# Kernel tuning notes

Measured on AMD Instinct MI355X. Metric: run time of the kernel, lower is better.

The kernel has to match this reference:

```python
import jax, jax.numpy as jnp
import numpy as np

B, C, H, W = 2, 256, 64, 64
CQ = C // 8  # query/key channels in PAM


def setup_inputs() -> dict:
    key = jax.random.key(0)
    ks = jax.random.split(key, 16)
    s = lambda *sh: sh
    inp = {
        'r_f': jax.random.normal(ks[0], (B, C, H, W), jnp.float32),
        'g_f': jax.random.normal(ks[1], (B, C, H, W), jnp.float32),
        'b_f': jax.random.normal(ks[2], (B, C, H, W), jnp.float32),
        'a_f': jax.random.normal(ks[3], (B, C, H, W), jnp.float32),
        # PAM params (1x1 convs)
        'Wq': jax.random.normal(ks[4], (CQ, C), jnp.float32) * (2.0 / C) ** 0.5,
        'bq': jnp.zeros((CQ,), jnp.float32),
        'Wk': jax.random.normal(ks[5], (CQ, C), jnp.float32) * (2.0 / C) ** 0.5,
        'bk': jnp.zeros((CQ,), jnp.float32),
        'Wv': jax.random.normal(ks[6], (C, C), jnp.float32) * (2.0 / C) ** 0.5,
        'bv': jnp.zeros((C,), jnp.float32),
        'gamma_pam': jax.random.normal(ks[7], (1,), jnp.float32) * 0.1,
        'gamma_cam': jax.random.normal(ks[8], (1,), jnp.float32) * 0.1,
        # 3x3 conv (shared across the 4 streams)
        'Wd': jax.random.normal(ks[9], (C, C, 3, 3), jnp.float32) * (2.0 / (C * 9)) ** 0.5,
        'bd': jnp.zeros((C,), jnp.float32),
    }
    return inp


def _pam(x, Wq, bq, Wk, bk, Wv, bv, gamma):
    # x: [B,C,H,W]
    b, c, h, w = x.shape
    n = h * w
    q = jnp.einsum('oc,bchw->bohw', Wq, x) + bq[None, :, None, None]  # [B,CQ,H,W]
    k = jnp.einsum('oc,bchw->bohw', Wk, x) + bk[None, :, None, None]
    v = jnp.einsum('oc,bchw->bohw', Wv, x) + bv[None, :, None, None]  # [B,C,H,W]
    q = q.reshape(b, -1, n)  # [B,CQ,N]
    k = k.reshape(b, -1, n)
    v = v.reshape(b, c, n)
    energy = jnp.einsum('bcn,bcm->bnm', q, k)            # [B,N,N]
    att = jax.nn.softmax(energy, axis=-1)
    out = jnp.einsum('bcm,bnm->bcn', v, att).reshape(b, c, h, w)
    return gamma * out + x


def _cam_att(x):
    b, c, h, w = x.shape
    v = x.reshape(b, c, h * w)
    energy = jnp.einsum('bcn,bdn->bcd', v, v)            # [B,C,C]
    energy_new = jnp.max(energy, axis=-1, keepdims=True) - energy
    return jax.nn.softmax(energy_new, axis=-1)


def _forward(r_f, g_f, b_f, a_f, Wq, bq, Wk, bk, Wv, bv, gamma_pam, gamma_cam, Wd, bd):
    xs = jnp.stack([r_f, g_f, b_f, a_f])                 # [4,B,C,H,W]
    s, b, c, h, w = xs.shape
    n = h * w
    sp = jax.vmap(lambda x: _pam(x, Wq, bq, Wk, bk, Wv, bv, gamma_pam))(xs)
    att = jax.vmap(_cam_att)(xs)                         # [4,B,C,C]
    # Each stream s accumulates cam_use(x_s, att_t) over all 4 attentions t:
    # sum_t (gamma*att_t@V_s + x_s) = gamma*(sum_t att_t)@V_s + 4*x_s
    att_sum = att.sum(axis=0)                            # [B,C,C]
    V = xs.reshape(s, b, c, n)
    sc = gamma_cam * jnp.einsum('bcd,sbdn->sbcn', att_sum, V).reshape(s, b, c, h, w) + 4.0 * xs
    y = sp + sc                                          # [4,B,C,H,W]
    y = y.reshape(s * b, c, h, w)
    y = jax.lax.conv_general_dilated(y, Wd, (1, 1), 'SAME',
                                     dimension_numbers=('NCHW', 'OIHW', 'NCHW'))
    y = y + bd[None, :, None, None]
    y = y.reshape(s, b, c, h, w)
    return (y[0], y[1], y[2], y[3])


def reference(r_f, g_f, b_f, a_f, Wq, bq, Wk, bk, Wv, bv, gamma_pam, gamma_cam, Wd, bd):
    return _forward(r_f, g_f, b_f, a_f, Wq, bq, Wk, bk, Wv, bv, gamma_pam, gamma_cam, Wd, bd)
```

## Files before the change

### kernel.cpp

```cpp
#include <hip/hip_runtime.h>


#define HW 4096

typedef unsigned short u16;
typedef __attribute__((ext_vector_type(4))) float f32x4;
typedef __attribute__((ext_vector_type(8))) short bf16x8;
typedef __attribute__((ext_vector_type(4))) unsigned u32x4;
typedef __attribute__((ext_vector_type(8))) unsigned short u16x8;
typedef __attribute__((ext_vector_type(4))) unsigned short u16x4;

__device__ __forceinline__ float bf2f(u16 u) { return __uint_as_float(((unsigned)u) << 16); }
__device__ __forceinline__ u16 f2bf(float f) {
    unsigned x = __float_as_uint(f);
    return (u16)((x + 0x7fffu + ((x >> 16) & 1u)) >> 16);
}
__device__ __forceinline__ void gload16(const void* g, void* l) {
    __builtin_amdgcn_global_load_lds((const __attribute__((address_space(1))) void*)g,
                                     (__attribute__((address_space(3))) void*)l, 16, 0, 0);
}
__device__ __forceinline__ unsigned cvtpk(float lo, float hi) {
    unsigned r;
    asm("v_cvt_pk_bf16_f32 %0, %1, %2" : "=v"(r) : "v"(lo), "v"(hi));
    return r;
}

struct XPtrs { const float* p[4]; };

enum { PM_QK = 0, PM_V = 1, PM_CAM = 2, PM_CONV = 3 };

template<int MODE>
__global__ __launch_bounds__(256)
void mfma_p_k(const u16* __restrict__ A, const u16* __restrict__ Bp,
              void* __restrict__ Cp,
              const float* __restrict__ b0, const float* __restrict__ b1,
              const float* __restrict__ gscale, XPtrs xs,
              int K, int lda, long aBatch, long bBatch, long cBatch, int sb0)
{
    const int n0 = blockIdx.x * 128, m0 = blockIdx.y * 128, z = blockIdx.z;
    const u16* Ab = A + (MODE == PM_CAM ? (size_t)(z & 1) * aBatch : (size_t)z * aBatch)
                      + (size_t)m0 * lda;
    const u16* Bb = Bp + (size_t)z * bBatch + (size_t)n0 * 8;

    __shared__ u16 As[4096];
    __shared__ u16 Bs[4096];

    const int t = threadIdx.x, lane = t & 63, w = t >> 6;
    const int mw = (w >> 1) * 64, nw = (w & 1) * 64;
    const int l15 = lane & 15, l4 = lane >> 4;

    f32x4 acc[4][4] = {};

    const u16* gaw = Ab + (size_t)lane * lda + w * 8;
    const u16* gbw = Bb + (size_t)w * (HW * 8) + (size_t)lane * 8;

    for (int kb = 0; kb < K; kb += 32) {
        gload16(gaw + kb,                    &As[w * 1024]);
        gload16(gaw + kb + (size_t)64 * lda, &As[w * 1024 + 512]);
        const u16* gb = gbw + (size_t)(kb >> 3) * (HW * 8);
        gload16(gb,       &Bs[w * 1024]);
        gload16(gb + 512, &Bs[w * 1024 + 512]);
        __syncthreads();

        bf16x8 af[4], bf[4];
        #pragma unroll
        for (int i = 0; i < 4; ++i) {
            af[i] = *(const bf16x8*)&As[l4 * 1024 + (mw + i * 16 + l15) * 8];
            bf[i] = *(const bf16x8*)&Bs[l4 * 1024 + (nw + i * 16 + l15) * 8];
        }
        #pragma unroll
        for (int mi = 0; mi < 4; ++mi)
            #pragma unroll
            for (int ni = 0; ni < 4; ++ni)
                acc[mi][ni] = __builtin_amdgcn_mfma_f32_16x16x32_bf16(af[mi], bf[ni], acc[mi][ni], 0, 0, 0);
        __syncthreads();
    }

    #pragma unroll
    for (int mi = 0; mi < 4; ++mi) {
        #pragma unroll
        for (int ni = 0; ni < 4; ++ni) {
            #pragma unroll
            for (int r = 0; r < 4; ++r) {
                const int row = m0 + mw + mi * 16 + l4 * 4 + r;
                const int col = n0 + nw + ni * 16 + l15;
                float v = acc[mi][ni][r];
                if constexpr (MODE == PM_QK) {
                    if (row < 64) {
                        v += (row < 32) ? b0[row] : b1[row - 32];
                        ((u16*)Cp)[(size_t)z * cBatch + (size_t)row * HW + col] = f2bf(v);
                    }
                } else if constexpr (MODE == PM_V) {
                    v += b0[row];
                    ((u16*)Cp)[(size_t)z * cBatch
                               + (((size_t)(col >> 3) * 256 + row) << 3) + (col & 7)] = f2bf(v);
                } else if constexpr (MODE == PM_CAM) {
                    const float* xb = xs.p[z >> 1] + (size_t)(z & 1) * (256 * HW);
                    v = gscale[0] * v + 5.f * xb[(size_t)row * HW + col];
                    ((float*)Cp)[(size_t)z * cBatch + (size_t)row * HW + col] = v;
                } else {
                    v += b0[row];
                    ((float*)Cp)[(size_t)(sb0 + z) * cBatch + (size_t)row * HW + col] = v;
                }
            }
        }
    }
}

__global__ __launch_bounds__(512, 4)
void flash_k(const u16* __restrict__ QKt, const u16* __restrict__ Vp,
             float* __restrict__ Yt, const float* __restrict__ gscale)
{
    __shared__ u16 Vs[32768];

    const int sb = blockIdx.y;
    const int t = threadIdx.x, w = t >> 6, lane = t & 63;
    const int l15 = lane & 15, l4 = lane >> 4;
    const int q0 = blockIdx.x * 128 + w * 16;

    const u16* QKb = QKt + (size_t)sb * ((size_t)HW * 64);
    const u16* Vb  = Vp + (size_t)sb * ((size_t)256 * HW);
    float* Yb = Yt + (size_t)sb * ((size_t)HW * 256);

    const bf16x8 aq = *(const bf16x8*)&QKb[(size_t)(q0 + l15) * 64 + l4 * 8];

    f32x4 acc[16] = {};
    float lrun = 0.f;
    const f32x4 zero4 = {0.f, 0.f, 0.f, 0.f};

    const int idxA = (l15 + ((lane & 16) << 1)) << 2;
    const int idxB = idxA + (16 << 2);
    const bool jhi = (lane & 32) != 0;

    for (int it = 0; it < 32; ++it) {
        __syncthreads();

        const u16* vsrc = Vb + (size_t)it * 32768;
        #pragma unroll
        for (int i = 0; i < 8; ++i)
            gload16(vsrc + i * 4096 + t * 8, &Vs[i * 4096 + t * 8]);

        const int m0 = it * 128;
        unsigned pk[16];
        float tsum = 0.f;
        #pragma unroll
        for (int j = 0; j < 8; ++j) {
            const bf16x8 bk = *(const bf16x8*)&QKb[(size_t)(m0 + j * 16 + l15) * 64 + 32 + l4 * 8];
            const f32x4 sj = __builtin_amdgcn_mfma_f32_16x16x32_bf16(bk, aq, zero4, 0, 0, 0);
            const float e0 = __expf(sj[0]);
            const float e1 = __expf(sj[1]);
            const float e2 = __expf(sj[2]);
            const float e3 = __expf(sj[3]);
            tsum += (e0 + e1) + (e2 + e3);
            pk[2 * j]     = cvtpk(e0, e1);
            pk[2 * j + 1] = cvtpk(e2, e3);
        }
        tsum += __shfl_xor(tsum, 16);
        tsum += __shfl_xor(tsum, 32);
        lrun += tsum;

        __syncthreads();

        #pragma unroll
        for (int ks = 0; ks < 4; ++ks) {
            u32x4 D;
            {
                const unsigned a0 = __builtin_amdgcn_ds_bpermute(idxA, (int)pk[4 * ks + 0]);
                const unsigned b0_ = __builtin_amdgcn_ds_bpermute(idxA, (int)pk[4 * ks + 2]);
                D[0] = jhi ? b0_ : a0;
                const unsigned a1 = __builtin_amdgcn_ds_bpermute(idxA, (int)pk[4 * ks + 1]);
                const unsigned b1_ = __builtin_amdgcn_ds_bpermute(idxA, (int)pk[4 * ks + 3]);
                D[1] = jhi ? b1_ : a1;
                const unsigned a2 = __builtin_amdgcn_ds_bpermute(idxB, (int)pk[4 * ks + 0]);
                const unsigned b2_ = __builtin_amdgcn_ds_bpermute(idxB, (int)pk[4 * ks + 2]);
                D[2] = jhi ? b2_ : a2;
                const unsigned a3 = __builtin_amdgcn_ds_bpermute(idxB, (int)pk[4 * ks + 1]);
                const unsigned b3_ = __builtin_amdgcn_ds_bpermute(idxB, (int)pk[4 * ks + 3]);
                D[3] = jhi ? b3_ : a3;
            }
            const bf16x8 ap = __builtin_bit_cast(bf16x8, D);
            #pragma unroll
            for (int ct = 0; ct < 16; ++ct) {
                const bf16x8 bv = *(const bf16x8*)&Vs[(4 * ks + l4) * 2048 + (ct * 16 + l15) * 8];
                acc[ct] = __builtin_amdgcn_mfma_f32_16x16x32_bf16(ap, bv, acc[ct], 0, 0, 0);
            }
        }
    }

    const float gp = gscale[0];
    #pragma unroll
    for (int r = 0; r < 4; ++r) {
        const int srcl = ((lane & 48) | (l4 * 4 + r)) << 2;
        const float lr = __int_as_float(__builtin_amdgcn_ds_bpermute(srcl, __float_as_int(lrun)));
        const float sc = gp / lr;
        const int row = q0 + l4 * 4 + r;
        #pragma unroll
        for (int ct = 0; ct < 16; ++ct)
            Yb[(size_t)row * 256 + ct * 16 + l15] = acc[ct][r] * sc;
    }
}

__global__ __launch_bounds__(256)
void xpack_k(XPtrs xs, u16* __restrict__ Xp)
{
    __shared__ float tile[64][65];
    const int sb = blockIdx.z;
    const int n0 = blockIdx.x * 64, c0 = blockIdx.y * 64;
    const float* X = xs.p[sb >> 1] + (size_t)(sb & 1) * (256 * HW);
    u16* Xo = Xp + (size_t)sb * ((size_t)32 * HW * 8);
    const int t = threadIdx.x;
    {
        const int c = t >> 2, p = t & 3;
        const float4* s4 = (const float4*)&X[(size_t)(c0 + c) * HW + n0 + p * 16];
        #pragma unroll
        for (int i = 0; i < 4; ++i) {
            const float4 v = s4[i];
            tile[c][p * 16 + i * 4 + 0] = v.x;
            tile[c][p * 16 + i * 4 + 1] = v.y;
            tile[c][p * 16 + i * 4 + 2] = v.z;
            tile[c][p * 16 + i * 4 + 3] = v.w;
        }
    }
    __syncthreads();
    const int n = t >> 2;
    #pragma unroll
    for (int pp = 0; pp < 2; ++pp) {
        const int cg = (t & 3) * 2 + pp;
        u16 o[8];
        #pragma unroll
        for (int cl = 0; cl < 8; ++cl) o[cl] = f2bf(tile[cg * 8 + cl][n]);
        *(u16x8*)&Xo[(((size_t)(c0 >> 3) + cg) * HW + (n0 + n)) * 8] = *(u16x8*)o;
    }
}

__global__ __launch_bounds__(256)
void tqkT_k(const u16* __restrict__ src, u16* __restrict__ dst)
{
    __shared__ u16 tile[64][72];
    const int sb = blockIdx.y;
    const int n0 = blockIdx.x * 64;
    const u16* s = src + (size_t)sb * (64 * HW);
    u16* d = dst + (size_t)sb * (HW * 64);
    const int t = threadIdx.x;
    #pragma unroll
    for (int p = 0; p < 2; ++p) {
        const int c = (t >> 3) + p * 32, nn = (t & 7) * 8;
        const u16x8 v = *(const u16x8*)&s[(size_t)c * HW + n0 + nn];
        *(u16x8*)&tile[c][nn] = v;
    }
    __syncthreads();
    const int n = t >> 2, co = (t & 3) * 16;
    u16 o[16];
    #pragma unroll
    for (int j = 0; j < 16; ++j) o[j] = tile[co + j][n];
    *(u16x8*)&d[(size_t)(n0 + n) * 64 + co]     = *(u16x8*)&o[0];
    *(u16x8*)&d[(size_t)(n0 + n) * 64 + co + 8] = *(u16x8*)&o[8];
}

__global__ __launch_bounds__(256)
void gram_k(float* __restrict__ Gp, XPtrs xs)
{
    const int bx = blockIdx.x, by = blockIdx.y, bz = blockIdx.z;
    const int sbi = bz & 7;
    const int n0 = bx * 64, m0 = by * 64;
    const int t = threadIdx.x;
    const int tm = t >> 4, tn = t & 15;
    const float* xb = xs.p[sbi >> 1] + (size_t)(sbi & 1) * (256 * HW) + (bz >> 3) * 512;

    __shared__ float As[16][68];
    __shared__ float Bs[16][68];
    float acc[4][4] = {};

    for (int kb = 0; kb < 512; kb += 16) {
        {
            const int m = t >> 2, k0 = (t & 3) * 4;
            float4 v = *(const float4*)(xb + (size_t)(m0 + m) * HW + (kb + k0));
            As[k0 + 0][m] = v.x; As[k0 + 1][m] = v.y; As[k0 + 2][m] = v.z; As[k0 + 3][m] = v.w;
        }
        {
            const int n = t >> 2, k0 = (t & 3) * 4;
            float4 v = *(const float4*)(xb + (size_t)(n0 + n) * HW + (kb + k0));
            Bs[k0 + 0][n] = v.x; Bs[k0 + 1][n] = v.y; Bs[k0 + 2][n] = v.z; Bs[k0 + 3][n] = v.w;
        }
        __syncthreads();
        #pragma unroll
        for (int k = 0; k < 16; ++k) {
            const float4 a = *(const float4*)&As[k][tm * 4];
            const float4 b = *(const float4*)&Bs[k][tn * 4];
            acc[0][0] += a.x * b.x; acc[0][1] += a.x * b.y; acc[0][2] += a.x * b.z; acc[0][3] += a.x * b.w;
            acc[1][0] += a.y * b.x; acc[1][1] += a.y * b.y; acc[1][2] += a.y * b.z; acc[1][3] += a.y * b.w;
            acc[2][0] += a.z * b.x; acc[2][1] += a.z * b.y; acc[2][2] += a.z * b.z; acc[2][3] += a.z * b.w;
            acc[3][0] += a.w * b.x; acc[3][1] += a.w * b.y; acc[3][2] += a.w * b.z; acc[3][3] += a.w * b.w;
        }
        __syncthreads();
    }
    float* Cf = Gp + (size_t)bz * 65536;
    #pragma unroll
    for (int i = 0; i < 4; ++i) {
        const int m = m0 + tm * 4 + i;
        *(float4*)&Cf[(size_t)m * 256 + n0 + tn * 4] =
            make_float4(acc[i][0], acc[i][1], acc[i][2], acc[i][3]);
    }
}

__global__ __launch_bounds__(256)
void greduce_k(const float* __restrict__ Gp, float* __restrict__ G)
{
    const size_t i = (size_t)blockIdx.x * 256 + threadIdx.x;
    float s = 0.f;
    #pragma unroll
    for (int sp = 0; sp < 8; ++sp) s += Gp[(size_t)sp * 524288 + i];
    G[i] = s;
}

__global__ __launch_bounds__(256)
void cam_softmax_k(const float* __restrict__ G, float* __restrict__ attsum)
{
    __shared__ float rmn[4], rsm[4];
    const int c = blockIdx.x, b = blockIdx.y;
    const int d = threadIdx.x;
    float acc = 0.f;
    for (int s = 0; s < 4; ++s) {
        const float* row = G + (((size_t)(s * 2 + b)) * 256 + c) * 256;
        const float e = row[d];
        float mn = e;
        for (int o = 32; o; o >>= 1) mn = fminf(mn, __shfl_down(mn, o));
        if ((d & 63) == 0) rmn[d >> 6] = mn;
        __syncthreads();
        mn = fminf(fminf(rmn[0], rmn[1]), fminf(rmn[2], rmn[3]));
        const float ex = __expf(mn - e);
        float sm = ex;
        for (int o = 32; o; o >>= 1) sm += __shfl_down(sm, o);
        if ((d & 63) == 0) rsm[d >> 6] = sm;
        __syncthreads();
        sm = rsm[0] + rsm[1] + rsm[2] + rsm[3];
        acc += ex * (1.0f / sm);
        __syncthreads();
    }
    attsum[((size_t)b * 256 + c) * 256 + d] = acc;
}

__global__ __launch_bounds__(256)
void transT_k(const float* __restrict__ Yt, float* __restrict__ Y)
{
    __shared__ float tile[64][65];
    const int sb = blockIdx.z;
    const int n0 = blockIdx.x * 64, c0 = blockIdx.y * 64;
    const float* src = Yt + (size_t)sb * ((size_t)HW * 256);
    float* dst = Y + (size_t)sb * ((size_t)256 * HW);
    const int t = threadIdx.x;
    {
        const int n = t >> 2, p = t & 3;
        const float4* s4 = (const float4*)&src[(size_t)(n0 + n) * 256 + c0 + p * 16];
        #pragma unroll
        for (int i = 0; i < 4; ++i) {
            const float4 v = s4[i];
            tile[n][p * 16 + i * 4 + 0] = v.x;
            tile[n][p * 16 + i * 4 + 1] = v.y;
            tile[n][p * 16 + i * 4 + 2] = v.z;
            tile[n][p * 16 + i * 4 + 3] = v.w;
        }
    }
    __syncthreads();
    const int c = t >> 2, p = t & 3;
    #pragma unroll
    for (int i = 0; i < 4; ++i) {
        float* dp = &dst[(size_t)(c0 + c) * HW + n0 + p * 16 + i * 4];
        float4 cur = *(float4*)dp;
        cur.x += tile[p * 16 + i * 4 + 0][c];
        cur.y += tile[p * 16 + i * 4 + 1][c];
        cur.z += tile[p * 16 + i * 4 + 2][c];
        cur.w += tile[p * 16 + i * 4 + 3][c];
        *(float4*)dp = cur;
    }
}

__global__ __launch_bounds__(256)
void im2col_k(const float* __restrict__ Y, u16* __restrict__ col, int sb0)
{
    const int n = blockIdx.x * 256 + threadIdx.x;
    const int kg = blockIdx.y;
    const int sbl = blockIdx.z;
    const float* Yb = Y + (size_t)(sb0 + sbl) * ((size_t)256 * HW);
    const int h = n >> 6, wc = n & 63;
    u16 out[8];
    #pragma unroll
    for (int kl = 0; kl < 8; ++kl) {
        const int k = kg * 8 + kl;
        const int ic = k / 9, r = k - ic * 9;
        const int ih = h + r / 3 - 1, iw = wc + (r % 3) - 1;
        float v = 0.f;
        if (ih >= 0 && ih < 64 && iw >= 0 && iw < 64)
            v = Yb[(size_t)ic * HW + (ih << 6) + iw];
        out[kl] = f2bf(v);
    }
    *(u16x8*)&col[(((size_t)sbl * 288 + kg) * HW + n) * 8] = *(u16x8*)out;
}

__global__ __launch_bounds__(256)
void cvt_k(const float* __restrict__ s, u16* __restrict__ d)
{
    const size_t i = ((size_t)blockIdx.x * 256 + threadIdx.x) * 4;
    const float4 v = *(const float4*)&s[i];
    u16 o[4] = { f2bf(v.x), f2bf(v.y), f2bf(v.z), f2bf(v.w) };
    *(u16x4*)&d[i] = *(u16x4*)o;
}

extern "C" void kernel_launch(void* const* d_in, const int* in_sizes, int n_in,
                              void* d_out, int out_size, void* d_ws, size_t ws_size,
                              hipStream_t stream)
{
    XPtrs xs;
    xs.p[0] = (const float*)d_in[0];
    xs.p[1] = (const float*)d_in[1];
    xs.p[2] = (const float*)d_in[2];
    xs.p[3] = (const float*)d_in[3];
    const float* Wq = (const float*)d_in[4];
    const float* bq = (const float*)d_in[5];
    const float* Wk = (const float*)d_in[6];
    const float* bk = (const float*)d_in[7];
    const float* Wv = (const float*)d_in[8];
    const float* bv = (const float*)d_in[9];
    const float* gp = (const float*)d_in[10];
    const float* gc = (const float*)d_in[11];
    const float* Wd = (const float*)d_in[12];
    const float* bd = (const float*)d_in[13];

    char* base = (char*)d_ws;
    size_t off = 0;
    auto alloc = [&](size_t bytes) -> char* {
        char* p = base + off;
        off = (off + bytes + 255) & ~(size_t)255;
        return p;
    };

    float* Y    = (float*)alloc((size_t)8 * 256 * HW * 4);
    u16*   Wdh  = (u16*)  alloc((size_t)256 * 2304 * 2);
    const size_t overlayStart = off;
    u16*   Xp   = (u16*)  alloc((size_t)8 * 32 * HW * 8 * 2);
    u16*   Vp   = (u16*)  alloc((size_t)8 * 256 * HW * 2);
    float* Yt   = (float*)alloc((size_t)8 * HW * 256 * 4);
    u16*   QKc  = (u16*)  alloc((size_t)8 * 64 * HW * 2);
    u16*   QKt  = (u16*)  alloc((size_t)8 * HW * 64 * 2);
    float* Gp   = (float*)alloc((size_t)64 * 65536 * 4);
    float* G    = (float*)alloc((size_t)8 * 65536 * 4);
    float* att  = (float*)alloc((size_t)2 * 65536 * 4);
    u16*   attH = (u16*)  alloc((size_t)2 * 65536 * 2);
    u16*   Wqkh = (u16*)  alloc((size_t)128 * 256 * 2);
    u16*   Wvh  = (u16*)  alloc((size_t)256 * 256 * 2);

    const size_t colPer = (size_t)288 * HW * 8 * 2;
    u16* colp = (u16*)(base + overlayStart);
    long nchunkL = (long)((ws_size - overlayStart) / colPer);
    const int nchunk = (int)(nchunkL > 8 ? 8 : (nchunkL < 1 ? 1 : nchunkL));

    dim3 T(256);

    xpack_k<<<dim3(64, 4, 8), T, 0, stream>>>(xs, Xp);
    cvt_k<<<dim3(8),   T, 0, stream>>>(Wq, Wqkh);
    cvt_k<<<dim3(8),   T, 0, stream>>>(Wk, Wqkh + 32 * 256);
    cvt_k<<<dim3(64),  T, 0, stream>>>(Wv, Wvh);
    cvt_k<<<dim3(576), T, 0, stream>>>(Wd, Wdh);

    gram_k<<<dim3(4, 4, 64), T, 0, stream>>>(Gp, xs);
    greduce_k<<<dim3(2048), T, 0, stream>>>(Gp, G);
    cam_softmax_k<<<dim3(256, 2), T, 0, stream>>>(G, att);
    cvt_k<<<dim3(128), T, 0, stream>>>(att, attH);

    mfma_p_k<PM_QK><<<dim3(32, 1, 8), T, 0, stream>>>(Wqkh, Xp, QKc, bq, bk, nullptr, xs,
                                                      256, 256, 0, (long)32 * HW * 8, (long)64 * HW, 0);
    tqkT_k<<<dim3(64, 8), T, 0, stream>>>(QKc, QKt);
    mfma_p_k<PM_V><<<dim3(32, 2, 8), T, 0, stream>>>(Wvh, Xp, Vp, bv, nullptr, nullptr, xs,
                                                     256, 256, 0, (long)32 * HW * 8, (long)256 * HW, 0);

    flash_k<<<dim3(32, 8), dim3(512), 0, stream>>>(QKt, Vp, Yt, gp);

    mfma_p_k<PM_CAM><<<dim3(32, 2, 8), T, 0, stream>>>(attH, Xp, Y, nullptr, nullptr, gc, xs,
                                                       256, 256, 65536, (long)32 * HW * 8, (long)256 * HW, 0);

    transT_k<<<dim3(64, 4, 8), T, 0, stream>>>(Yt, Y);

    for (int c0 = 0; c0 < 8; c0 += nchunk) {
        const int cs = (8 - c0 < nchunk) ? (8 - c0) : nchunk;
        im2col_k<<<dim3(16, 288, cs), T, 0, stream>>>(Y, colp, c0);
        mfma_p_k<PM_CONV><<<dim3(32, 2, cs), T, 0, stream>>>(Wdh, colp, d_out, bd, nullptr, nullptr, xs,
                                                             2304, 2304, 0, (long)288 * HW * 8, (long)256 * HW, c0);
    }
}
```

Measured before the change: 460.6 us.

## Compute CAM Gram matrix with split-bf16 MFMA instead of FP32 FMA

Replaces the scalar FP32 Gram kernel with an MFMA kernel that uses hi/lo bf16 splits (three products) to approximate FP32 accuracy. The split operands are produced by xpack in a K-major packed layout and reuse the V buffer's memory. This moves the main cost of the channel Gram computation onto the matrix cores, at the price of extra bytes written in xpack and slightly reduced precision from dropping the lo*lo term.

```diff
diff --git a/kernel.cpp b/kernel.cpp
--- a/kernel.cpp
+++ b/kernel.cpp
@@ -107,6 +107,71 @@
     }
 }
 
+__global__ __launch_bounds__(256)
+void gramm_k(const u16* __restrict__ Hi, const u16* __restrict__ Lo,
+             float* __restrict__ Gp)
+{
+    const int n0 = blockIdx.x * 128, m0 = blockIdx.y * 128, bz = blockIdx.z;
+    const int sb = bz & 7, sp = bz >> 3;
+    const u16* Hb = Hi + (size_t)sb * 1048576;
+    const u16* Lb = Lo + (size_t)sb * 1048576;
+
+    __shared__ u16 AsH[4096], AsL[4096], BsH[4096], BsL[4096];
+
+    const int t = threadIdx.x, lane = t & 63, w = t >> 6;
+    const int mw = (w >> 1) * 64, nw = (w & 1) * 64;
+    const int l15 = lane & 15, l4 = lane >> 4;
+
+    f32x4 acc[4][4] = {};
+
+    for (int kb = sp * 512; kb < sp * 512 + 512; kb += 32) {
+        const size_t g = (size_t)(kb >> 3) + w;
+        const u16* hA = Hb + g * 2048 + (size_t)(m0 + lane) * 8;
+        const u16* lA = Lb + g * 2048 + (size_t)(m0 + lane) * 8;
+        const u16* hB = Hb + g * 2048 + (size_t)(n0 + lane) * 8;
+        const u16* lB = Lb + g * 2048 + (size_t)(n0 + lane) * 8;
+        gload16(hA,       &AsH[w * 1024]);
+        gload16(hA + 512, &AsH[w * 1024 + 512]);
+        gload16(lA,       &AsL[w * 1024]);
+        gload16(lA + 512, &AsL[w * 1024 + 512]);
+        gload16(hB,       &BsH[w * 1024]);
+        gload16(hB + 512, &BsH[w * 1024 + 512]);
+        gload16(lB,       &BsL[w * 1024]);
+        gload16(lB + 512, &BsL[w * 1024 + 512]);
+        __syncthreads();
+
+        bf16x8 ah[4], al[4], bh[4], bl[4];
+        #pragma unroll
+        for (int i = 0; i < 4; ++i) {
+            ah[i] = *(const bf16x8*)&AsH[l4 * 1024 + (mw + i * 16 + l15) * 8];
+            al[i] = *(const bf16x8*)&AsL[l4 * 1024 + (mw + i * 16 + l15) * 8];
+            bh[i] = *(const bf16x8*)&BsH[l4 * 1024 + (nw + i * 16 + l15) * 8];
+            bl[i] = *(const bf16x8*)&BsL[l4 * 1024 + (nw + i * 16 + l15) * 8];
+        }
+        #pragma unroll
+        for (int mi = 0; mi < 4; ++mi)
+            #pragma unroll
+            for (int ni = 0; ni < 4; ++ni) {
+                acc[mi][ni] = __builtin_amdgcn_mfma_f32_16x16x32_bf16(ah[mi], bh[ni], acc[mi][ni], 0, 0, 0);
+                acc[mi][ni] = __builtin_amdgcn_mfma_f32_16x16x32_bf16(ah[mi], bl[ni], acc[mi][ni], 0, 0, 0);
+                acc[mi][ni] = __builtin_amdgcn_mfma_f32_16x16x32_bf16(al[mi], bh[ni], acc[mi][ni], 0, 0, 0);
+            }
+        __syncthreads();
+    }
+
+    float* Cf = Gp + (size_t)bz * 65536;
+    #pragma unroll
+    for (int mi = 0; mi < 4; ++mi)
+        #pragma unroll
+        for (int ni = 0; ni < 4; ++ni)
+            #pragma unroll
+            for (int r = 0; r < 4; ++r) {
+                const int row = m0 + mw + mi * 16 + l4 * 4 + r;
+                const int col = n0 + nw + ni * 16 + l15;
+                Cf[(size_t)row * 256 + col] = acc[mi][ni][r];
+            }
+}
+
 __global__ __launch_bounds__(512, 4)
 void flash_k(const u16* __restrict__ QKt, const u16* __restrict__ Vp,
              float* __restrict__ Yt, const float* __restrict__ gscale)
@@ -201,7 +266,8 @@
 }
 
 __global__ __launch_bounds__(256)
-void xpack_k(XPtrs xs, u16* __restrict__ Xp)
+void xpack_k(XPtrs xs, u16* __restrict__ Xp,
+             u16* __restrict__ XpGhi, u16* __restrict__ XpGlo)
 {
     __shared__ float tile[64][65];
     const int sb = blockIdx.z;
@@ -222,14 +288,36 @@
         }
     }
     __syncthreads();
-    const int n = t >> 2;
-    #pragma unroll
-    for (int pp = 0; pp < 2; ++pp) {
-        const int cg = (t & 3) * 2 + pp;
-        u16 o[8];
-        #pragma unroll
-        for (int cl = 0; cl < 8; ++cl) o[cl] = f2bf(tile[cg * 8 + cl][n]);
-        *(u16x8*)&Xo[(((size_t)(c0 >> 3) + cg) * HW + (n0 + n)) * 8] = *(u16x8*)o;
+    {
+        const int n = t >> 2;
+        #pragma unroll
+        for (int pp = 0; pp < 2; ++pp) {
+            const int cg = (t & 3) * 2 + pp;
+            u16 o[8];
+            #pragma unroll
+            for (int cl = 0; cl < 8; ++cl) o[cl] = f2bf(tile[cg * 8 + cl][n]);
+            *(u16x8*)&Xo[(((size_t)(c0 >> 3) + cg) * HW + (n0 + n)) * 8] = *(u16x8*)o;
+        }
+    }
+    {
+        const int cl = t & 63, kgl = t >> 6;
+        u16* Hb = XpGhi + (size_t)sb * 1048576;
+        u16* Lb = XpGlo + (size_t)sb * 1048576;
+        #pragma unroll
+        for (int q = 0; q < 2; ++q) {
+            const int kg = kgl + q * 4;
+            u16 hi8[8], lo8[8];
+            #pragma unroll
+            for (int j = 0; j < 8; ++j) {
+                const float v = tile[cl][kg * 8 + j];
+                const u16 h = f2bf(v);
+                hi8[j] = h;
+                lo8[j] = f2bf(v - bf2f(h));
+            }
+            const size_t o = (((size_t)(n0 >> 3) + kg) * 256 + (c0 + cl)) * 8;
+            *(u16x8*)&Hb[o] = *(u16x8*)hi8;
+            *(u16x8*)&Lb[o] = *(u16x8*)lo8;
+        }
     }
 }
 
@@ -255,52 +343,6 @@
     for (int j = 0; j < 16; ++j) o[j] = tile[co + j][n];
     *(u16x8*)&d[(size_t)(n0 + n) * 64 + co]     = *(u16x8*)&o[0];
     *(u16x8*)&d[(size_t)(n0 + n) * 64 + co + 8] = *(u16x8*)&o[8];
-}
-
-__global__ __launch_bounds__(256)
-void gram_k(float* __restrict__ Gp, XPtrs xs)
-{
-    const int bx = blockIdx.x, by = blockIdx.y, bz = blockIdx.z;
-    const int sbi = bz & 7;
-    const int n0 = bx * 64, m0 = by * 64;
-    const int t = threadIdx.x;
-    const int tm = t >> 4, tn = t & 15;
-    const float* xb = xs.p[sbi >> 1] + (size_t)(sbi & 1) * (256 * HW) + (bz >> 3) * 512;
-
-    __shared__ float As[16][68];
-    __shared__ float Bs[16][68];
-    float acc[4][4] = {};
-
-    for (int kb = 0; kb < 512; kb += 16) {
-        {
-            const int m = t >> 2, k0 = (t & 3) * 4;
-            float4 v = *(const float4*)(xb + (size_t)(m0 + m) * HW + (kb + k0));
-            As[k0 + 0][m] = v.x; As[k0 + 1][m] = v.y; As[k0 + 2][m] = v.z; As[k0 + 3][m] = v.w;
-        }
-        {
-            const int n = t >> 2, k0 = (t & 3) * 4;
-            float4 v = *(const float4*)(xb + (size_t)(n0 + n) * HW + (kb + k0));
-            Bs[k0 + 0][n] = v.x; Bs[k0 + 1][n] = v.y; Bs[k0 + 2][n] = v.z; Bs[k0 + 3][n] = v.w;
-        }
-        __syncthreads();
-        #pragma unroll
-        for (int k = 0; k < 16; ++k) {
-            const float4 a = *(const float4*)&As[k][tm * 4];
-            const float4 b = *(const float4*)&Bs[k][tn * 4];
-            acc[0][0] += a.x * b.x; acc[0][1] += a.x * b.y; acc[0][2] += a.x * b.z; acc[0][3] += a.x * b.w;
-            acc[1][0] += a.y * b.x; acc[1][1] += a.y * b.y; acc[1][2] += a.y * b.z; acc[1][3] += a.y * b.w;
-            acc[2][0] += a.z * b.x; acc[2][1] += a.z * b.y; acc[2][2] += a.z * b.z; acc[2][3] += a.z * b.w;
-            acc[3][0] += a.w * b.x; acc[3][1] += a.w * b.y; acc[3][2] += a.w * b.z; acc[3][3] += a.w * b.w;
-        }
-        __syncthreads();
-    }
-    float* Cf = Gp + (size_t)bz * 65536;
-    #pragma unroll
-    for (int i = 0; i < 4; ++i) {
-        const int m = m0 + tm * 4 + i;
-        *(float4*)&Cf[(size_t)m * 256 + n0 + tn * 4] =
-            make_float4(acc[i][0], acc[i][1], acc[i][2], acc[i][3]);
-    }
 }
 
 __global__ __launch_bounds__(256)
@@ -438,16 +480,18 @@
     u16*   Wdh  = (u16*)  alloc((size_t)256 * 2304 * 2);
     const size_t overlayStart = off;
     u16*   Xp   = (u16*)  alloc((size_t)8 * 32 * HW * 8 * 2);
-    u16*   Vp   = (u16*)  alloc((size_t)8 * 256 * HW * 2);
-    float* Yt   = (float*)alloc((size_t)8 * HW * 256 * 4);
-    u16*   QKc  = (u16*)  alloc((size_t)8 * 64 * HW * 2);
-    u16*   QKt  = (u16*)  alloc((size_t)8 * HW * 64 * 2);
     float* Gp   = (float*)alloc((size_t)64 * 65536 * 4);
     float* G    = (float*)alloc((size_t)8 * 65536 * 4);
     float* att  = (float*)alloc((size_t)2 * 65536 * 4);
     u16*   attH = (u16*)  alloc((size_t)2 * 65536 * 2);
+    float* Yt   = (float*)alloc((size_t)8 * HW * 256 * 4);
+    u16*   QKc  = (u16*)  alloc((size_t)8 * 64 * HW * 2);
+    u16*   QKt  = (u16*)  alloc((size_t)8 * HW * 64 * 2);
     u16*   Wqkh = (u16*)  alloc((size_t)128 * 256 * 2);
     u16*   Wvh  = (u16*)  alloc((size_t)256 * 256 * 2);
+    u16*   XpGhi = (u16*) alloc((size_t)8 * 1048576 * 2);
+    u16*   XpGlo = (u16*) alloc((size_t)8 * 1048576 * 2);
+    u16*   Vp    = XpGhi;
 
     const size_t colPer = (size_t)288 * HW * 8 * 2;
     u16* colp = (u16*)(base + overlayStart);
@@ -456,13 +500,13 @@
 
     dim3 T(256);
 
-    xpack_k<<<dim3(64, 4, 8), T, 0, stream>>>(xs, Xp);
+    xpack_k<<<dim3(64, 4, 8), T, 0, stream>>>(xs, Xp, XpGhi, XpGlo);
     cvt_k<<<dim3(8),   T, 0, stream>>>(Wq, Wqkh);
     cvt_k<<<dim3(8),   T, 0, stream>>>(Wk, Wqkh + 32 * 256);
     cvt_k<<<dim3(64),  T, 0, stream>>>(Wv, Wvh);
     cvt_k<<<dim3(576), T, 0, stream>>>(Wd, Wdh);
 
-    gram_k<<<dim3(4, 4, 64), T, 0, stream>>>(Gp, xs);
+    gramm_k<<<dim3(2, 2, 64), T, 0, stream>>>(XpGhi, XpGlo, Gp);
     greduce_k<<<dim3(2048), T, 0, stream>>>(Gp, G);
     cam_softmax_k<<<dim3(256, 2), T, 0, stream>>>(G, att);
     cvt_k<<<dim3(128), T, 0, stream>>>(att, attH);
```

After: 436.2 us. 5.3% less time.
